# Kernel optimization log

Hardware: AMD Instinct MI355X
Metric: run time of the kernel (lower is better)

The kernel has to match this reference:

```python
import jax, jax.numpy as jnp
import numpy as np

B, H, S, D = 4, 16, 2048, 64
NEG = -1000000000.0


def setup_inputs() -> dict:
    key = jax.random.key(0)
    kq, kk, kv, km = jax.random.split(key, 4)
    Q = jax.random.normal(kq, (B, H, S, D), dtype=jnp.float32)
    K = jax.random.normal(kk, (B, H, S, D), dtype=jnp.float32)
    V = jax.random.normal(kv, (B, H, S, D), dtype=jnp.float32)
    attn_mask = jax.random.randint(km, (B, 1, 1, S), 0, 2).astype(jnp.bool_)
    return {"Q": Q, "K": K, "V": V, "attn_mask": attn_mask}


def reference(Q, K, V, attn_mask):
    scale = 1.0 / (Q.shape[-1] ** 0.5)
    # [B,H,S,S] scores, masked, softmax over keys
    scores = jnp.einsum("bhqd,bhkd->bhqk", Q, K) * scale
    scores = jnp.where(attn_mask, NEG, scores)
    attn_prob = jax.nn.softmax(scores, axis=-1)
    context = jnp.einsum("bhqk,bhkd->bhqd", attn_prob, V)
    return context
```

## Files before the change

### kernel.cpp

```cpp
#include <hip/hip_runtime.h>
#include <hip/hip_bf16.h>

#define B_ 4
#define H_ 16
#define S_ 2048
#define D_ 64
#define BH_ (B_ * H_)
#define VSTR 2048

#define QS 0.18033688011112042f

typedef __bf16 bf16_t;
typedef __attribute__((ext_vector_type(8))) bf16_t bf16x8;
typedef __attribute__((ext_vector_type(4))) bf16_t bf16x4;
typedef __attribute__((ext_vector_type(4))) float f32x4;

#if __has_builtin(__builtin_amdgcn_exp2f)
#define EX2(x) __builtin_amdgcn_exp2f(x)
#else
#define EX2(x) exp2f(x)
#endif

#define KC_OFF 0u
#define VT_OFF 16777216u
#define CIDX_OFF 33554432u
#define NK_OFF 33619968u

__device__ __forceinline__ bf16x4 cvt4(const float4 a) {
  return (bf16x4){(bf16_t)a.x, (bf16_t)a.y, (bf16_t)a.z, (bf16_t)a.w};
}

__global__ __launch_bounds__(256) void scan_kernel(const unsigned char* __restrict__ raw,
                                                   int* __restrict__ cidx,
                                                   int* __restrict__ nkarr) {
  const int b = blockIdx.x;
  const int tid = threadIdx.x;
  __shared__ int isBool;
  if (tid == 0) isBool = 0;
  __syncthreads();
  int any = 0;
  for (int i = tid; i < B_ * S_; i += 256)
    if ((i & 3) && raw[i]) any = 1;
  if (any) isBool = 1;
  __syncthreads();
  const bool ib = (isBool != 0);

  int flags[8], cnt = 0;
  const int base = tid * 8;
#pragma unroll
  for (int j = 0; j < 8; ++j) {
    const int key = base + j;
    const int m = ib ? (raw[b * S_ + key] ? 1 : 0)
                     : (((const int*)raw)[b * S_ + key] ? 1 : 0);
    flags[j] = m ? 0 : 1;
    cnt += flags[j];
  }
  __shared__ int sc[256];
  sc[tid] = cnt;
  __syncthreads();
  for (int off = 1; off < 256; off <<= 1) {
    const int v = sc[tid];
    const int u = (tid >= off) ? sc[tid - off] : 0;
    __syncthreads();
    sc[tid] = v + u;
    __syncthreads();
  }
  int pos = (tid > 0) ? sc[tid - 1] : 0;
  const int total = sc[255];
  int* cb = cidx + b * VSTR;
#pragma unroll
  for (int j = 0; j < 8; ++j)
    if (flags[j]) cb[pos++] = base + j;
  if (tid == 0) nkarr[b] = total;
  const int padend = ((total + 63) >> 6) << 6;
  for (int i = total + tid; i < padend; i += 256) cb[i] = 0;
}

__global__ __launch_bounds__(256) void gather_kernel(const float* __restrict__ K,
                                                     const float* __restrict__ V,
                                                     const int* __restrict__ cidx,
                                                     const int* __restrict__ nkarr,
                                                     bf16_t* __restrict__ Kc,
                                                     bf16_t* __restrict__ Vtc) {
  const int blk = blockIdx.x;
  const int bh = blk >> 5, tile = blk & 31;
  const int b = bh >> 4;
  if (tile * 64 >= nkarr[b]) return;
  const int tid = threadIdx.x;
  __shared__ int idx[64];
  __shared__ float T[64][65];
  if (tid < 64) idx[tid] = cidx[b * VSTR + tile * 64 + tid];
  __syncthreads();
  {
    const int row = tid >> 2, g = tid & 3;
    const float* src = K + (size_t)bh * S_ * D_ + (size_t)idx[row] * D_;
    bf16_t* dst = Kc + (size_t)bh * VSTR * D_ + (size_t)(tile * 64 + row) * D_;
#pragma unroll
    for (int c = 0; c < 2; ++c) {
      const float4 lo = *(const float4*)(src + c * 32 + g * 4);
      const float4 hi = *(const float4*)(src + c * 32 + 16 + g * 4);
      *(bf16x4*)(dst + (c * 4 + g) * 8) = cvt4(lo);
      *(bf16x4*)(dst + (c * 4 + g) * 8 + 4) = cvt4(hi);
    }
  }
  const float* vsrc = V + (size_t)bh * S_ * D_;
#pragma unroll
  for (int rep = 0; rep < 4; ++rep) {
    const int i2 = rep * 256 + tid;
    const int row = i2 >> 4, d4 = (i2 & 15) << 2;
    const float4 v = *(const float4*)(vsrc + (size_t)idx[row] * D_ + d4);
    T[row][d4] = v.x; T[row][d4 + 1] = v.y; T[row][d4 + 2] = v.z; T[row][d4 + 3] = v.w;
  }
  __syncthreads();
  bf16_t* vdst = Vtc + (size_t)bh * D_ * VSTR + tile * 64;
#pragma unroll
  for (int rep = 0; rep < 4; ++rep) {
    const int i2 = rep * 256 + tid;
    const int d = i2 >> 4, k4 = (i2 & 15) << 2;
    const int kc = k4 >> 5, within = k4 & 31;
    const int g = (within & 15) >> 2, half = (within & 16) ? 4 : 0;
    const int pos = (kc * 4 + g) * 8 + half;
    const bf16x4 o = {(bf16_t)T[k4][d], (bf16_t)T[k4 + 1][d], (bf16_t)T[k4 + 2][d],
                      (bf16_t)T[k4 + 3][d]};
    *(bf16x4*)(vdst + (size_t)d * VSTR + pos) = o;
  }
}


__device__ __forceinline__ bf16x8 qpack(const float4 a, const float4 b) {
  bf16x8 r;
  r[0] = (bf16_t)(a.x * QS); r[1] = (bf16_t)(a.y * QS);
  r[2] = (bf16_t)(a.z * QS); r[3] = (bf16_t)(a.w * QS);
  r[4] = (bf16_t)(b.x * QS); r[5] = (bf16_t)(b.y * QS);
  r[6] = (bf16_t)(b.z * QS); r[7] = (bf16_t)(b.w * QS);
  return r;
}

__global__ __launch_bounds__(512, 4) void attn_main_kernel(const float* __restrict__ Q,
                                                           const bf16_t* __restrict__ Kc,
                                                           const bf16_t* __restrict__ Vtc,
                                                           const int* __restrict__ nkarr,
                                                           float* __restrict__ out) {
  __shared__ bf16_t Kl[2][64][64];
  __shared__ bf16_t Vl[2][64][64];

  const int bid = blockIdx.x;
  const int wu = (bid & 7) * 64 + (bid >> 3);
  const int qt = wu & 7, bh = wu >> 3, b = bh >> 4;

  const int nk = nkarr[b];
  const int nt = (nk + 63) >> 6;

  const int tid = threadIdx.x, wid = tid >> 6, lane = tid & 63;
  const int gg = (lane >> 4) & 3, g4 = gg << 2, qi = lane & 15;
  const int q7 = qi & 7;
  const int koff0 = ((gg) ^ q7) << 3;
  const int koff1 = ((4 + gg) ^ q7) << 3;

  const size_t bhoff = (size_t)bh * (S_ * D_);
  const bf16_t* Kg = Kc + (size_t)bh * VSTR * D_;
  const bf16_t* Vg = Vtc + (size_t)bh * D_ * VSTR;

  const int qrow0 = qt * 256 + wid * 32 + qi;
  bf16x8 qb[2][2];
#pragma unroll
  for (int g = 0; g < 2; ++g) {
    const float* qp = Q + bhoff + (size_t)(qrow0 + g * 16) * D_;
#pragma unroll
    for (int c = 0; c < 2; ++c)
      qb[g][c] = qpack(*(const float4*)(qp + c * 32 + g4),
                       *(const float4*)(qp + c * 32 + 16 + g4));
  }

  const int srow = tid >> 3;
  const int scc = tid & 7;
  const int soff = ((scc ^ (srow & 7)) << 3);
  const bf16_t* Kgs = Kg + (size_t)srow * D_ + scc * 8;
  const bf16_t* Vgs = Vg + (size_t)srow * VSTR + scc * 8;

  {
    const uint4 k0 = *(const uint4*)Kgs;
    const uint4 v0 = *(const uint4*)Vgs;
    *(uint4*)&Kl[0][srow][soff] = k0;
    *(uint4*)&Vl[0][srow][soff] = v0;
  }
  __syncthreads();

  f32x4 o[2][4];
#pragma unroll
  for (int g = 0; g < 2; ++g)
#pragma unroll
    for (int dt = 0; dt < 4; ++dt) o[g][dt] = (f32x4){0.f, 0.f, 0.f, 0.f};
  float lrun0 = 0.f, lrun1 = 0.f;

  for (int t = 0; t < nt; ++t) {
    const int cur = t & 1;
    const int nxt = cur ^ 1;
    const bool more = (t + 1 < nt);
    const int kv = (t + 1) * 64;
    const int rem = nk - t * 64;

    uint4 k0, v0;
    if (more) {
      k0 = *(const uint4*)(Kgs + (size_t)kv * D_);
      v0 = *(const uint4*)(Vgs + kv);
    }

    bf16x8 pb0[2], pb1[2];
    float ts0 = 0.f, ts1 = 0.f;
    __builtin_amdgcn_s_setprio(1);
#pragma unroll
    for (int kt = 0; kt < 4; ++kt) {
      const bf16_t* krow = &Kl[cur][kt * 16 + qi][0];
      f32x4 a0 = {0.f, 0.f, 0.f, 0.f}, a1 = a0;
      {
        const bf16x8 ka = *(const bf16x8*)(krow + koff0);
        a0 = __builtin_amdgcn_mfma_f32_16x16x32_bf16(ka, qb[0][0], a0, 0, 0, 0);
        a1 = __builtin_amdgcn_mfma_f32_16x16x32_bf16(ka, qb[1][0], a1, 0, 0, 0);
      }
      {
        const bf16x8 ka = *(const bf16x8*)(krow + koff1);
        a0 = __builtin_amdgcn_mfma_f32_16x16x32_bf16(ka, qb[0][1], a0, 0, 0, 0);
        a1 = __builtin_amdgcn_mfma_f32_16x16x32_bf16(ka, qb[1][1], a1, 0, 0, 0);
      }
      if (more) {
#pragma unroll
        for (int r = 0; r < 4; ++r) {
          const float p0 = EX2(a0[r]);
          const float p1 = EX2(a1[r]);
          ts0 += p0; ts1 += p1;
          pb0[kt >> 1][(kt & 1) * 4 + r] = (bf16_t)p0;
          pb1[kt >> 1][(kt & 1) * 4 + r] = (bf16_t)p1;
        }
      } else {
#pragma unroll
        for (int r = 0; r < 4; ++r) {
          const int kidx = kt * 16 + g4 + r;
          float p0 = EX2(a0[r]);
          float p1 = EX2(a1[r]);
          p0 = (kidx < rem) ? p0 : 0.f;
          p1 = (kidx < rem) ? p1 : 0.f;
          ts0 += p0; ts1 += p1;
          pb0[kt >> 1][(kt & 1) * 4 + r] = (bf16_t)p0;
          pb1[kt >> 1][(kt & 1) * 4 + r] = (bf16_t)p1;
        }
      }
    }
    __builtin_amdgcn_s_setprio(0);
    lrun0 += ts0;
    lrun1 += ts1;

    if (more) *(uint4*)&Kl[nxt][srow][soff] = k0;

    __builtin_amdgcn_s_setprio(1);
#pragma unroll
    for (int dt = 0; dt < 4; ++dt) {
      const bf16_t* vrow = &Vl[cur][dt * 16 + qi][0];
      {
        const bf16x8 va = *(const bf16x8*)(vrow + koff0);
        o[0][dt] = __builtin_amdgcn_mfma_f32_16x16x32_bf16(va, pb0[0], o[0][dt], 0, 0, 0);
        o[1][dt] = __builtin_amdgcn_mfma_f32_16x16x32_bf16(va, pb1[0], o[1][dt], 0, 0, 0);
      }
      {
        const bf16x8 va = *(const bf16x8*)(vrow + koff1);
        o[0][dt] = __builtin_amdgcn_mfma_f32_16x16x32_bf16(va, pb0[1], o[0][dt], 0, 0, 0);
        o[1][dt] = __builtin_amdgcn_mfma_f32_16x16x32_bf16(va, pb1[1], o[1][dt], 0, 0, 0);
      }
    }
    __builtin_amdgcn_s_setprio(0);

    if (more) {
      *(uint4*)&Vl[nxt][srow][soff] = v0;
      __syncthreads();
    }
  }

#pragma unroll
  for (int g = 0; g < 2; ++g) {
    float lr = g ? lrun1 : lrun0;
    lr += __shfl_xor(lr, 16);
    lr += __shfl_xor(lr, 32);
    const float inv = 1.0f / lr;
    float* op = out + bhoff + (size_t)(qrow0 + g * 16) * D_;
#pragma unroll
    for (int dt = 0; dt < 4; ++dt) {
      float4 w;
      w.x = o[g][dt][0] * inv;
      w.y = o[g][dt][1] * inv;
      w.z = o[g][dt][2] * inv;
      w.w = o[g][dt][3] * inv;
      *(float4*)(op + dt * 16 + g4) = w;
    }
  }
}

extern "C" void kernel_launch(void* const* d_in, const int* in_sizes, int n_in,
                              void* d_out, int out_size, void* d_ws, size_t ws_size,
                              hipStream_t stream) {
  const float* Q = (const float*)d_in[0];
  const float* K = (const float*)d_in[1];
  const float* V = (const float*)d_in[2];
  const unsigned char* mraw = (const unsigned char*)d_in[3];
  float* out = (float*)d_out;

  char* ws = (char*)d_ws;
  bf16_t* Kc = (bf16_t*)(ws + KC_OFF);
  bf16_t* Vtc = (bf16_t*)(ws + VT_OFF);
  int* cidx = (int*)(ws + CIDX_OFF);
  int* nkarr = (int*)(ws + NK_OFF);

  scan_kernel<<<B_, 256, 0, stream>>>(mraw, cidx, nkarr);
  gather_kernel<<<BH_ * 32, 256, 0, stream>>>(K, V, cidx, nkarr, Kc, Vtc);
  attn_main_kernel<<<512, 512, 0, stream>>>(Q, Kc, Vtc, nkarr, out);
}
```

Baseline: 71.55 us.

## Load K/V fragments directly from global memory instead of LDS double-buffering

Removes the shared-memory double buffer and block-wide barriers, so each wave loads its K and V MFMA operands straight from global memory, relying on L1/L2 for reuse across waves. Blocks shrink from 512 to 256 threads and the grid doubles, with 128 query rows per block. This removes LDS traffic and synchronisation but repeats global/cache loads per wave and exposes load latency with no explicit prefetch.

```diff
diff --git a/kernel.cpp b/kernel.cpp
--- a/kernel.cpp
+++ b/kernel.cpp
@@ -136,32 +136,26 @@
   return r;
 }
 
-__global__ __launch_bounds__(512, 4) void attn_main_kernel(const float* __restrict__ Q,
+__global__ __launch_bounds__(256, 4) void attn_main_kernel(const float* __restrict__ Q,
                                                            const bf16_t* __restrict__ Kc,
                                                            const bf16_t* __restrict__ Vtc,
                                                            const int* __restrict__ nkarr,
                                                            float* __restrict__ out) {
-  __shared__ bf16_t Kl[2][64][64];
-  __shared__ bf16_t Vl[2][64][64];
-
   const int bid = blockIdx.x;
-  const int wu = (bid & 7) * 64 + (bid >> 3);
-  const int qt = wu & 7, bh = wu >> 3, b = bh >> 4;
+  const int wu = (bid & 7) * 128 + (bid >> 3);
+  const int qt = wu & 15, bh = wu >> 4, b = bh >> 4;
 
   const int nk = nkarr[b];
   const int nt = (nk + 63) >> 6;
 
   const int tid = threadIdx.x, wid = tid >> 6, lane = tid & 63;
   const int gg = (lane >> 4) & 3, g4 = gg << 2, qi = lane & 15;
-  const int q7 = qi & 7;
-  const int koff0 = ((gg) ^ q7) << 3;
-  const int koff1 = ((4 + gg) ^ q7) << 3;
 
   const size_t bhoff = (size_t)bh * (S_ * D_);
-  const bf16_t* Kg = Kc + (size_t)bh * VSTR * D_;
-  const bf16_t* Vg = Vtc + (size_t)bh * D_ * VSTR;
-
-  const int qrow0 = qt * 256 + wid * 32 + qi;
+  const bf16_t* Kgl = Kc + (size_t)bh * VSTR * D_ + (size_t)qi * D_;
+  const bf16_t* Vgl = Vtc + (size_t)bh * D_ * VSTR + (size_t)qi * VSTR;
+
+  const int qrow0 = qt * 128 + wid * 32 + qi;
   bf16x8 qb[2][2];
 #pragma unroll
   for (int g = 0; g < 2; ++g) {
@@ -172,20 +166,6 @@
                        *(const float4*)(qp + c * 32 + 16 + g4));
   }
 
-  const int srow = tid >> 3;
-  const int scc = tid & 7;
-  const int soff = ((scc ^ (srow & 7)) << 3);
-  const bf16_t* Kgs = Kg + (size_t)srow * D_ + scc * 8;
-  const bf16_t* Vgs = Vg + (size_t)srow * VSTR + scc * 8;
-
-  {
-    const uint4 k0 = *(const uint4*)Kgs;
-    const uint4 v0 = *(const uint4*)Vgs;
-    *(uint4*)&Kl[0][srow][soff] = k0;
-    *(uint4*)&Vl[0][srow][soff] = v0;
-  }
-  __syncthreads();
-
   f32x4 o[2][4];
 #pragma unroll
   for (int g = 0; g < 2; ++g)
@@ -193,86 +173,78 @@
     for (int dt = 0; dt < 4; ++dt) o[g][dt] = (f32x4){0.f, 0.f, 0.f, 0.f};
   float lrun0 = 0.f, lrun1 = 0.f;
 
+  const int cc0 = gg * 8;
+  const int cc1 = 32 + gg * 8;
+
   for (int t = 0; t < nt; ++t) {
-    const int cur = t & 1;
-    const int nxt = cur ^ 1;
     const bool more = (t + 1 < nt);
-    const int kv = (t + 1) * 64;
     const int rem = nk - t * 64;
-
-    uint4 k0, v0;
-    if (more) {
-      k0 = *(const uint4*)(Kgs + (size_t)kv * D_);
-      v0 = *(const uint4*)(Vgs + kv);
+    const int kv = t * 64;
+
+    f32x4 s0[4], s1[4];
+    __builtin_amdgcn_s_setprio(1);
+#pragma unroll
+    for (int kt = 0; kt < 4; ++kt) {
+      const bf16_t* kp = Kgl + (size_t)(kv + kt * 16) * D_;
+      const bf16x8 ka0 = *(const bf16x8*)(kp + cc0);
+      const bf16x8 ka1 = *(const bf16x8*)(kp + cc1);
+      f32x4 a0 = {0.f, 0.f, 0.f, 0.f}, a1 = a0;
+      a0 = __builtin_amdgcn_mfma_f32_16x16x32_bf16(ka0, qb[0][0], a0, 0, 0, 0);
+      a1 = __builtin_amdgcn_mfma_f32_16x16x32_bf16(ka0, qb[1][0], a1, 0, 0, 0);
+      a0 = __builtin_amdgcn_mfma_f32_16x16x32_bf16(ka1, qb[0][1], a0, 0, 0, 0);
+      a1 = __builtin_amdgcn_mfma_f32_16x16x32_bf16(ka1, qb[1][1], a1, 0, 0, 0);
+      s0[kt] = a0; s1[kt] = a1;
+    }
+    __builtin_amdgcn_s_setprio(0);
+
+    bf16x8 va[4][2];
+#pragma unroll
+    for (int dt = 0; dt < 4; ++dt) {
+      const bf16_t* vp = Vgl + (size_t)(dt * 16) * VSTR + kv;
+      va[dt][0] = *(const bf16x8*)(vp + cc0);
+      va[dt][1] = *(const bf16x8*)(vp + cc1);
     }
 
     bf16x8 pb0[2], pb1[2];
     float ts0 = 0.f, ts1 = 0.f;
-    __builtin_amdgcn_s_setprio(1);
-#pragma unroll
-    for (int kt = 0; kt < 4; ++kt) {
-      const bf16_t* krow = &Kl[cur][kt * 16 + qi][0];
-      f32x4 a0 = {0.f, 0.f, 0.f, 0.f}, a1 = a0;
-      {
-        const bf16x8 ka = *(const bf16x8*)(krow + koff0);
-        a0 = __builtin_amdgcn_mfma_f32_16x16x32_bf16(ka, qb[0][0], a0, 0, 0, 0);
-        a1 = __builtin_amdgcn_mfma_f32_16x16x32_bf16(ka, qb[1][0], a1, 0, 0, 0);
-      }
-      {
-        const bf16x8 ka = *(const bf16x8*)(krow + koff1);
-        a0 = __builtin_amdgcn_mfma_f32_16x16x32_bf16(ka, qb[0][1], a0, 0, 0, 0);
-        a1 = __builtin_amdgcn_mfma_f32_16x16x32_bf16(ka, qb[1][1], a1, 0, 0, 0);
-      }
-      if (more) {
+    if (more) {
+#pragma unroll
+      for (int kt = 0; kt < 4; ++kt)
 #pragma unroll
         for (int r = 0; r < 4; ++r) {
-          const float p0 = EX2(a0[r]);
-          const float p1 = EX2(a1[r]);
+          const float p0 = EX2(s0[kt][r]);
+          const float p1 = EX2(s1[kt][r]);
           ts0 += p0; ts1 += p1;
           pb0[kt >> 1][(kt & 1) * 4 + r] = (bf16_t)p0;
           pb1[kt >> 1][(kt & 1) * 4 + r] = (bf16_t)p1;
         }
-      } else {
+    } else {
+#pragma unroll
+      for (int kt = 0; kt < 4; ++kt)
 #pragma unroll
         for (int r = 0; r < 4; ++r) {
           const int kidx = kt * 16 + g4 + r;
-          float p0 = EX2(a0[r]);
-          float p1 = EX2(a1[r]);
+          float p0 = EX2(s0[kt][r]);
+          float p1 = EX2(s1[kt][r]);
           p0 = (kidx < rem) ? p0 : 0.f;
           p1 = (kidx < rem) ? p1 : 0.f;
           ts0 += p0; ts1 += p1;
           pb0[kt >> 1][(kt & 1) * 4 + r] = (bf16_t)p0;
           pb1[kt >> 1][(kt & 1) * 4 + r] = (bf16_t)p1;
         }
-      }
-    }
-    __builtin_amdgcn_s_setprio(0);
+    }
     lrun0 += ts0;
     lrun1 += ts1;
 
-    if (more) *(uint4*)&Kl[nxt][srow][soff] = k0;
-
     __builtin_amdgcn_s_setprio(1);
 #pragma unroll
     for (int dt = 0; dt < 4; ++dt) {
-      const bf16_t* vrow = &Vl[cur][dt * 16 + qi][0];
-      {
-        const bf16x8 va = *(const bf16x8*)(vrow + koff0);
-        o[0][dt] = __builtin_amdgcn_mfma_f32_16x16x32_bf16(va, pb0[0], o[0][dt], 0, 0, 0);
-        o[1][dt] = __builtin_amdgcn_mfma_f32_16x16x32_bf16(va, pb1[0], o[1][dt], 0, 0, 0);
-      }
-      {
-        const bf16x8 va = *(const bf16x8*)(vrow + koff1);
-        o[0][dt] = __builtin_amdgcn_mfma_f32_16x16x32_bf16(va, pb0[1], o[0][dt], 0, 0, 0);
-        o[1][dt] = __builtin_amdgcn_mfma_f32_16x16x32_bf16(va, pb1[1], o[1][dt], 0, 0, 0);
-      }
+      o[0][dt] = __builtin_amdgcn_mfma_f32_16x16x32_bf16(va[dt][0], pb0[0], o[0][dt], 0, 0, 0);
+      o[1][dt] = __builtin_amdgcn_mfma_f32_16x16x32_bf16(va[dt][0], pb1[0], o[1][dt], 0, 0, 0);
+      o[0][dt] = __builtin_amdgcn_mfma_f32_16x16x32_bf16(va[dt][1], pb0[1], o[0][dt], 0, 0, 0);
+      o[1][dt] = __builtin_amdgcn_mfma_f32_16x16x32_bf16(va[dt][1], pb1[1], o[1][dt], 0, 0, 0);
     }
     __builtin_amdgcn_s_setprio(0);
-
-    if (more) {
-      *(uint4*)&Vl[nxt][srow][soff] = v0;
-      __syncthreads();
-    }
   }
 
 #pragma unroll
@@ -311,5 +283,5 @@
 
   scan_kernel<<<B_, 256, 0, stream>>>(mraw, cidx, nkarr);
   gather_kernel<<<BH_ * 32, 256, 0, stream>>>(K, V, cidx, nkarr, Kc, Vtc);
-  attn_main_kernel<<<512, 512, 0, stream>>>(Q, Kc, Vtc, nkarr, out);
-}
+  attn_main_kernel<<<1024, 256, 0, stream>>>(Q, Kc, Vtc, nkarr, out);
+}
```

After: 197.4 us. 176% more time.
